# Kernel tuning notes

Hardware: AMD Instinct MI355X
Metric: run time of the kernel (lower is better)

Reference implementation:

```python
import jax, jax.numpy as jnp
import numpy as np

N = 50000      # nodes
E = 800000     # edges (before self loops)
IN_D = 128
HID = 128
OUT_D = 64
HEADS = 4
FH = HID // HEADS  # per-head feature dim
NEG_SLOPE = 0.2


def setup_inputs() -> dict:
    key = jax.random.key(0)
    ks = jax.random.split(key, 16)
    s = 0.05
    inp = {
        "x": jax.random.normal(ks[0], (N, IN_D), dtype=jnp.float32),
        "edge_index": jax.random.randint(ks[1], (2, E), 0, N, dtype=jnp.int32),
        "Wi": jax.random.normal(ks[2], (IN_D, HID), dtype=jnp.float32) * s,
        "bi": jnp.zeros((HID,), dtype=jnp.float32),
        "W0": jax.random.normal(ks[3], (HID, HID), dtype=jnp.float32) * s,
        "as0": jax.random.normal(ks[4], (HEADS, FH), dtype=jnp.float32) * s,
        "ad0": jax.random.normal(ks[5], (HEADS, FH), dtype=jnp.float32) * s,
        "b0": jnp.zeros((HID,), dtype=jnp.float32),
        "W1": jax.random.normal(ks[6], (HID, HID), dtype=jnp.float32) * s,
        "as1": jax.random.normal(ks[7], (HEADS, FH), dtype=jnp.float32) * s,
        "ad1": jax.random.normal(ks[8], (HEADS, FH), dtype=jnp.float32) * s,
        "b1": jnp.zeros((HID,), dtype=jnp.float32),
        "Wo": jax.random.normal(ks[9], (HID, OUT_D), dtype=jnp.float32) * s,
        "bo": jnp.zeros((OUT_D,), dtype=jnp.float32),
    }
    return inp


def _gat_layer(h, src, dst, W, a_src, a_dst, b):
    # h: [N, HID]; src/dst: [E'] (with self loops)
    hp = (h @ W).reshape(N, HEADS, FH)               # projected per-head features
    al_s = jnp.einsum('nhf,hf->nh', hp, a_src)       # [N, H]
    al_d = jnp.einsum('nhf,hf->nh', hp, a_dst)
    e = jax.nn.leaky_relu(al_s[src] + al_d[dst], NEG_SLOPE)  # [E', H]
    # neighbor softmax over incoming edges of each dst node (stable)
    m = jax.ops.segment_max(e, dst, num_segments=N)
    m = jnp.where(jnp.isfinite(m), m, 0.0)
    num = jnp.exp(e - m[dst])
    den = jax.ops.segment_sum(num, dst, num_segments=N)
    coef = num / (den[dst] + 1e-16)                  # [E', H]
    out = jax.ops.segment_sum(coef[:, :, None] * hp[src], dst, num_segments=N)
    return out.reshape(N, HID) + b


def reference(x, edge_index, Wi, bi, W0, as0, ad0, b0, W1, as1, ad1, b1, Wo, bo):
    # add self loops (PyG GATConv default)
    loop = jnp.arange(N, dtype=edge_index.dtype)
    src = jnp.concatenate([edge_index[0], loop])
    dst = jnp.concatenate([edge_index[1], loop])

    h = jax.nn.relu(x @ Wi + bi)
    # layer 0 (dropout = identity in eval)
    h = h + jax.nn.relu(_gat_layer(h, src, dst, W0, as0, ad0, b0))
    # layer 1
    h = h + jax.nn.relu(_gat_layer(h, src, dst, W1, as1, ad1, b1))
    return h @ Wo + bo
```

## Files before the change

kernel.cpp:

```cpp
#include <hip/hip_runtime.h>
#include <hip/hip_bf16.h>


__device__ __forceinline__ float lrelu(float x){ return x > 0.f ? x : 0.2f * x; }

typedef __attribute__((ext_vector_type(8))) short bf16x8;
typedef __attribute__((ext_vector_type(4))) float f32x4;

__device__ __forceinline__ ushort f2bf(float f){
    union { __hip_bfloat16 b; ushort u; } cv;
    cv.b = __float2bfloat16(f);
    return cv.u;
}
__device__ __forceinline__ float bf2f(short u){
    union { uint i; float f; } c;
    c.i = ((uint)(ushort)u) << 16;
    return c.f;
}

constexpr int CAP = 64;
constexpr int BUCKET_CAP = 8192;
constexpr int P1_EDGES = 2048;

__global__ __launch_bounds__(256) void bin_edges_kernel(
    const int* __restrict__ ei, int* __restrict__ gcur, int2* __restrict__ binned, int E, int N)
{
    __shared__ int hist[256], offs[256], gpos[256];
    __shared__ int2 stag[P1_EDGES];
    __shared__ int wsum[4];
    int tid = threadIdx.x;
    hist[tid] = 0;
    __syncthreads();

    int base = blockIdx.x * P1_EDGES;
    int srcv[8], dstv[8], rk[8];
    #pragma unroll
    for (int j = 0; j < 8; j++){
        int e = base + j * 256 + tid;
        if (e < E + N){
            int s, d;
            if (e < E){ s = ei[e]; d = ei[E + e]; } else { s = e - E; d = s; }
            srcv[j] = s; dstv[j] = d;
            rk[j] = atomicAdd(&hist[d >> 8], 1);
        } else dstv[j] = -1;
    }
    __syncthreads();

    int lane = tid & 63, wid = tid >> 6;
    int v = hist[tid];
    int x = v;
    #pragma unroll
    for (int o = 1; o < 64; o <<= 1){ int t = __shfl_up(x, o); if (lane >= o) x += t; }
    if (lane == 63) wsum[wid] = x;
    __syncthreads();
    int woff = 0;
    for (int w2 = 0; w2 < wid; w2++) woff += wsum[w2];
    offs[tid] = woff + x - v;
    __syncthreads();

    #pragma unroll
    for (int j = 0; j < 8; j++){
        if (dstv[j] >= 0){
            int b = dstv[j] >> 8;
            stag[offs[b] + rk[j]] = make_int2(srcv[j], dstv[j]);
        }
    }
    if (hist[tid] > 0) gpos[tid] = atomicAdd(&gcur[tid], hist[tid]);
    __syncthreads();

    int nE = offs[255] + hist[255];
    for (int i = tid; i < nE; i += 256){
        int2 p = stag[i];
        int b = p.y >> 8;
        int idx = gpos[b] + (i - offs[b]);
        if (idx < BUCKET_CAP) binned[(size_t)b * BUCKET_CAP + idx] = p;
    }
}

__global__ __launch_bounds__(256) void build_slots_kernel(
    const int* __restrict__ gcur, const int2* __restrict__ binned,
    int* __restrict__ cnt, int* __restrict__ slots, int N)
{
    __shared__ int cnt_l[256];
    __shared__ int slots_l[256][CAP];
    int tid = threadIdx.x;
    int b = blockIdx.x;
    cnt_l[tid] = 0;
    __syncthreads();

    int ne = gcur[b]; if (ne > BUCKET_CAP) ne = BUCKET_CAP;
    const int2* bp = binned + (size_t)b * BUCKET_CAP;
    for (int i = tid; i < ne; i += 256){
        int2 p = bp[i];
        int ld = p.y & 255;
        int pos = atomicAdd(&cnt_l[ld], 1);
        if (pos < CAP) slots_l[ld][pos] = p.x;
    }
    __syncthreads();

    int node = b * 256 + tid;
    if (node < N) cnt[node] = min(cnt_l[tid], CAP);
    for (int j = tid; j < 256 * CAP; j += 256){
        int n2 = b * 256 + (j >> 6);
        if (n2 < N) slots[(size_t)n2 * CAP + (j & 63)] = slots_l[j >> 6][j & 63];
    }
}

__global__ void wcast_all_kernel(const float* __restrict__ Wi, const float* __restrict__ W0,
                                 const float* __restrict__ W1, const float* __restrict__ Wo,
                                 ushort* __restrict__ ti, ushort* __restrict__ t0,
                                 ushort* __restrict__ t1, ushort* __restrict__ to_){
    int i = blockIdx.x * 256 + threadIdx.x;
    if (i < 16384){
        int k = i >> 7, n = i & 127;        ti[n * 128 + k] = f2bf(Wi[i]);
    } else if (i < 32768){
        int j = i - 16384; int k = j >> 7, n = j & 127;  t0[n * 128 + k] = f2bf(W0[j]);
    } else if (i < 49152){
        int j = i - 32768; int k = j >> 7, n = j & 127;  t1[n * 128 + k] = f2bf(W1[j]);
    } else if (i < 57344){
        int j = i - 49152; int k = j / 64, n = j % 64;   to_[n * 128 + k] = f2bf(Wo[j]);
    }
}

template<int NCOL, bool RELU, bool BIAS, bool BF16OUT, bool LOGITS>
__global__ __launch_bounds__(256) void mfma_matmul_kernel(
    const float* __restrict__ A,
    const ushort* __restrict__ Wt,
    const float* __restrict__ bias,
    void* __restrict__ Cv,
    const float* __restrict__ as_, const float* __restrict__ ad_,
    float* __restrict__ als, float* __restrict__ ald, int M)
{
    constexpr int NT = NCOL / 16;
    __shared__ ushort Ws[NCOL][136];
    int tid = threadIdx.x;
    for (int i = tid * 8; i < NCOL * 128; i += 256 * 8){
        int r = i >> 7, c = i & 127;
        *(uint4*)&Ws[r][c] = *(const uint4*)&Wt[i];
    }
    __syncthreads();

    int lane = tid & 63, wave = tid >> 6;
    int r15 = lane & 15;
    int ko  = (lane >> 4) * 8;
    int row  = blockIdx.x * 64 + wave * 16 + r15;
    int rowc = row < M ? row : M - 1;
    const float* Arow = A + (size_t)rowc * 128;

    f32x4 acc[NT];
    #pragma unroll
    for (int t = 0; t < NT; t++) acc[t] = (f32x4){0.f, 0.f, 0.f, 0.f};

    #pragma unroll
    for (int kt = 0; kt < 4; ++kt){
        float4 a0 = *(const float4*)&Arow[kt * 32 + ko];
        float4 a1 = *(const float4*)&Arow[kt * 32 + ko + 4];
        bf16x8 af;
        af[0] = f2bf(a0.x); af[1] = f2bf(a0.y); af[2] = f2bf(a0.z); af[3] = f2bf(a0.w);
        af[4] = f2bf(a1.x); af[5] = f2bf(a1.y); af[6] = f2bf(a1.z); af[7] = f2bf(a1.w);
        #pragma unroll
        for (int t = 0; t < NT; t++){
            bf16x8 bf = *(const bf16x8*)&Ws[t * 16 + r15][kt * 32 + ko];
            acc[t] = __builtin_amdgcn_mfma_f32_16x16x32_bf16(af, bf, acc[t], 0, 0, 0);
        }
    }

    int oc    = lane & 15;
    int orow0 = blockIdx.x * 64 + wave * 16 + (lane >> 4) * 4;
    #pragma unroll
    for (int t = 0; t < NT; t++){
        int ocol = t * 16 + oc;
        float bv = BIAS ? bias[ocol] : 0.f;
        #pragma unroll
        for (int rg = 0; rg < 4; rg++){
            int orow = orow0 + rg;
            if (orow < M){
                float v = acc[t][rg] + bv;
                if (RELU) v = fmaxf(v, 0.f);
                if (BF16OUT) ((ushort*)Cv)[(size_t)orow * NCOL + ocol] = f2bf(v);
                else         ((float*)Cv) [(size_t)orow * NCOL + ocol] = v;
            }
        }
    }

    if (LOGITS){
        float sva[4][4], svd[4][4];
        #pragma unroll
        for (int hh = 0; hh < 4; hh++){
            float as0v = as_[hh*32 + oc],      ad0v = ad_[hh*32 + oc];
            float as1v = as_[hh*32 + 16 + oc], ad1v = ad_[hh*32 + 16 + oc];
            #pragma unroll
            for (int rg = 0; rg < 4; rg++){
                sva[hh][rg] = acc[2*hh][rg] * as0v + acc[2*hh+1][rg] * as1v;
                svd[hh][rg] = acc[2*hh][rg] * ad0v + acc[2*hh+1][rg] * ad1v;
            }
        }
        #pragma unroll
        for (int o = 1; o < 16; o <<= 1){
            #pragma unroll
            for (int hh = 0; hh < 4; hh++)
                #pragma unroll
                for (int rg = 0; rg < 4; rg++){
                    sva[hh][rg] += __shfl_xor(sva[hh][rg], o);
                    svd[hh][rg] += __shfl_xor(svd[hh][rg], o);
                }
        }
        if (oc < 4){
            #pragma unroll
            for (int rg = 0; rg < 4; rg++){
                int orow = orow0 + rg;
                if (orow < M){
                    float va = (oc & 2) ? ((oc & 1) ? sva[3][rg] : sva[2][rg])
                                        : ((oc & 1) ? sva[1][rg] : sva[0][rg]);
                    float vd = (oc & 2) ? ((oc & 1) ? svd[3][rg] : svd[2][rg])
                                        : ((oc & 1) ? svd[1][rg] : svd[0][rg]);
                    als[orow * 4 + oc] = va;
                    ald[orow * 4 + oc] = vd;
                }
            }
        }
    }
}

__global__ __launch_bounds__(256) void gat_aggregate_kernel(
    const int* __restrict__ cnt, const int* __restrict__ slots,
    const ushort* __restrict__ hp, const float* __restrict__ als,
    const float* __restrict__ ald, const float* __restrict__ bias,
    float* __restrict__ h, int n)
{
    __shared__ float num_s[4][CAP * 5];
    __shared__ int   src_s[4][CAP];
    int wid = threadIdx.x >> 6;
    int lane = threadIdx.x & 63;
    int node = blockIdx.x * 4 + wid;
    float* nums = num_s[wid];
    int*   srcs = src_s[wid];

    int deg = 0;
    float4 aldv = make_float4(0.f,0.f,0.f,0.f);
    if (node < n){
        deg = cnt[node];
        if (deg > CAP) deg = CAP;
        aldv = *(const float4*)&ald[node * 4];
    }

    float m0=-1e30f, m1=-1e30f, m2=-1e30f, m3=-1e30f;
    if (lane < deg){
        int s = slots[node * CAP + lane];
        srcs[lane] = s;
        float4 av = *(const float4*)&als[s * 4];
        m0 = lrelu(av.x + aldv.x);
        m1 = lrelu(av.y + aldv.y);
        m2 = lrelu(av.z + aldv.z);
        m3 = lrelu(av.w + aldv.w);
        nums[lane*5+0]=m0; nums[lane*5+1]=m1; nums[lane*5+2]=m2; nums[lane*5+3]=m3;
    }
    #pragma unroll
    for (int o = 1; o < 64; o <<= 1){
        m0=fmaxf(m0,__shfl_xor(m0,o)); m1=fmaxf(m1,__shfl_xor(m1,o));
        m2=fmaxf(m2,__shfl_xor(m2,o)); m3=fmaxf(m3,__shfl_xor(m3,o));
    }
    __syncthreads();

    float d0=0.f,d1=0.f,d2=0.f,d3=0.f;
    if (lane < deg){
        d0 = __expf(nums[lane*5+0]-m0);
        d1 = __expf(nums[lane*5+1]-m1);
        d2 = __expf(nums[lane*5+2]-m2);
        d3 = __expf(nums[lane*5+3]-m3);
        nums[lane*5+0]=d0; nums[lane*5+1]=d1; nums[lane*5+2]=d2; nums[lane*5+3]=d3;
    }
    #pragma unroll
    for (int o = 1; o < 64; o <<= 1){
        d0+=__shfl_xor(d0,o); d1+=__shfl_xor(d1,o);
        d2+=__shfl_xor(d2,o); d3+=__shfl_xor(d3,o);
    }
    float inv0=1.f/(d0+1e-16f), inv1=1.f/(d1+1e-16f);
    float inv2=1.f/(d2+1e-16f), inv3=1.f/(d3+1e-16f);
    __syncthreads();

    int er = lane >> 4;
    int fg = (lane & 15) * 8;
    int head = (lane & 15) >> 2;
    float inv = (head & 2) ? ((head & 1) ? inv3 : inv2)
                           : ((head & 1) ? inv1 : inv0);
    float a0=0.f,a1=0.f,a2=0.f,a3=0.f,a4=0.f,a5=0.f,a6=0.f,a7=0.f;
    for (int i = 0; i < deg; i += 4){
        int e = i + er;
        bool v = e < deg;
        int ec = v ? e : 0;
        int s = srcs[ec];
        float c = nums[ec*5 + head] * inv;
        c = v ? c : 0.f;
        bf16x8 hv = *(const bf16x8*)&hp[(size_t)s * 128 + fg];
        a0 = fmaf(c, bf2f(hv[0]), a0);
        a1 = fmaf(c, bf2f(hv[1]), a1);
        a2 = fmaf(c, bf2f(hv[2]), a2);
        a3 = fmaf(c, bf2f(hv[3]), a3);
        a4 = fmaf(c, bf2f(hv[4]), a4);
        a5 = fmaf(c, bf2f(hv[5]), a5);
        a6 = fmaf(c, bf2f(hv[6]), a6);
        a7 = fmaf(c, bf2f(hv[7]), a7);
    }
    a0 += __shfl_xor(a0,16); a0 += __shfl_xor(a0,32);
    a1 += __shfl_xor(a1,16); a1 += __shfl_xor(a1,32);
    a2 += __shfl_xor(a2,16); a2 += __shfl_xor(a2,32);
    a3 += __shfl_xor(a3,16); a3 += __shfl_xor(a3,32);
    a4 += __shfl_xor(a4,16); a4 += __shfl_xor(a4,32);
    a5 += __shfl_xor(a5,16); a5 += __shfl_xor(a5,32);
    a6 += __shfl_xor(a6,16); a6 += __shfl_xor(a6,32);
    a7 += __shfl_xor(a7,16); a7 += __shfl_xor(a7,32);

    if (node < n){
        float sA = (er & 2) ? ((er & 1) ? a6 : a4) : ((er & 1) ? a2 : a0);
        float sB = (er & 2) ? ((er & 1) ? a7 : a5) : ((er & 1) ? a3 : a1);
        int f2 = fg + er * 2;
        float r0 = fmaxf(sA + bias[f2],     0.f);
        float r1 = fmaxf(sB + bias[f2 + 1], 0.f);
        float* hp2 = &h[(size_t)node * 128 + f2];
        float2 old = *(float2*)hp2;
        *(float2*)hp2 = make_float2(old.x + r0, old.y + r1);
    }
}

extern "C" void kernel_launch(void* const* d_in, const int* in_sizes, int n_in,
                              void* d_out, int out_size, void* d_ws, size_t ws_size,
                              hipStream_t stream)
{
    const float* x   = (const float*)d_in[0];
    const int*   ei  = (const int*)d_in[1];
    const float* Wi  = (const float*)d_in[2];
    const float* bi  = (const float*)d_in[3];
    const float* W0  = (const float*)d_in[4];
    const float* as0 = (const float*)d_in[5];
    const float* ad0 = (const float*)d_in[6];
    const float* b0  = (const float*)d_in[7];
    const float* W1  = (const float*)d_in[8];
    const float* as1 = (const float*)d_in[9];
    const float* ad1 = (const float*)d_in[10];
    const float* b1  = (const float*)d_in[11];
    const float* Wo  = (const float*)d_in[12];
    const float* bo  = (const float*)d_in[13];
    float* out = (float*)d_out;

    int N = in_sizes[0] / 128;
    int E = in_sizes[1] / 2;
    int EN = E + N;
    int NB = (N + 255) >> 8;

    char* w = (char*)d_ws;
    float*  h     = (float*)w;  w += (size_t)N * 128 * 4;
    ushort* hpb   = (ushort*)w; w += (size_t)N * 128 * 2;
    float*  als   = (float*)w;  w += (size_t)N * 4 * 4;
    float*  ald   = (float*)w;  w += (size_t)N * 4 * 4;
    int*    cnt   = (int*)w;    w += (size_t)N * 4;
    w = (char*)(((uintptr_t)w + 255) & ~(uintptr_t)255);
    int*    slots = (int*)w;    w += (size_t)N * CAP * 4;
    w = (char*)(((uintptr_t)w + 255) & ~(uintptr_t)255);
    int*    gcur  = (int*)w;    w += 256 * 4;
    w = (char*)(((uintptr_t)w + 255) & ~(uintptr_t)255);
    int2*   binned= (int2*)w;   w += (size_t)NB * BUCKET_CAP * 8;
    w = (char*)(((uintptr_t)w + 255) & ~(uintptr_t)255);
    ushort* wt_i  = (ushort*)w; w += (size_t)128 * 128 * 2;
    ushort* wt_0  = (ushort*)w; w += (size_t)128 * 128 * 2;
    ushort* wt_1  = (ushort*)w; w += (size_t)128 * 128 * 2;
    ushort* wt_o  = (ushort*)w; w += (size_t)64  * 128 * 2;

    hipMemsetAsync(gcur, 0, 256 * 4, stream);
    bin_edges_kernel<<<(EN + P1_EDGES - 1) / P1_EDGES, 256, 0, stream>>>(ei, gcur, binned, E, N);
    build_slots_kernel<<<NB, 256, 0, stream>>>(gcur, binned, cnt, slots, N);

    wcast_all_kernel<<<224, 256, 0, stream>>>(Wi, W0, W1, Wo, wt_i, wt_0, wt_1, wt_o);

    int mgrid = (N + 63) / 64;
    int agrid = (N + 3) / 4;

    mfma_matmul_kernel<128, true, true, false, false><<<mgrid, 256, 0, stream>>>(
        x, wt_i, bi, h, nullptr, nullptr, nullptr, nullptr, N);

    mfma_matmul_kernel<128, false, false, true, true><<<mgrid, 256, 0, stream>>>(
        h, wt_0, nullptr, hpb, as0, ad0, als, ald, N);
    gat_aggregate_kernel<<<agrid, 256, 0, stream>>>(cnt, slots, hpb, als, ald, b0, h, N);

    mfma_matmul_kernel<128, false, false, true, true><<<mgrid, 256, 0, stream>>>(
        h, wt_1, nullptr, hpb, as1, ad1, als, ald, N);
    gat_aggregate_kernel<<<agrid, 256, 0, stream>>>(cnt, slots, hpb, als, ald, b1, h, N);

    mfma_matmul_kernel<64, false, true, false, false><<<mgrid, 256, 0, stream>>>(
        h, wt_o, bo, out, nullptr, nullptr, nullptr, nullptr, N);
}
```

Before: 184.6 us.

## Split each node's GAT aggregation across two wavefronts by feature half

Measured after the change: 263.9 us. 42.9% more time.

```diff
diff --git a/kernel.cpp b/kernel.cpp
--- a/kernel.cpp
+++ b/kernel.cpp
@@ -232,7 +232,8 @@
     __shared__ int   src_s[4][CAP];
     int wid = threadIdx.x >> 6;
     int lane = threadIdx.x & 63;
-    int node = blockIdx.x * 4 + wid;
+    int node = blockIdx.x * 2 + (wid >> 1);
+    int half = wid & 1;
     float* nums = num_s[wid];
     int*   srcs = src_s[wid];
 
@@ -260,7 +261,6 @@
         m0=fmaxf(m0,__shfl_xor(m0,o)); m1=fmaxf(m1,__shfl_xor(m1,o));
         m2=fmaxf(m2,__shfl_xor(m2,o)); m3=fmaxf(m3,__shfl_xor(m3,o));
     }
-    __syncthreads();
 
     float d0=0.f,d1=0.f,d2=0.f,d3=0.f;
     if (lane < deg){
@@ -277,22 +277,22 @@
     }
     float inv0=1.f/(d0+1e-16f), inv1=1.f/(d1+1e-16f);
     float inv2=1.f/(d2+1e-16f), inv3=1.f/(d3+1e-16f);
-    __syncthreads();
-
-    int er = lane >> 4;
-    int fg = (lane & 15) * 8;
-    int head = (lane & 15) >> 2;
-    float inv = (head & 2) ? ((head & 1) ? inv3 : inv2)
-                           : ((head & 1) ? inv1 : inv0);
+
+    int er = lane >> 3;
+    int li = lane & 7;
+    int FG = half * 64 + li * 8;
+    int head = half * 2 + (li >> 2);
+    float inv = half ? ((li & 4) ? inv3 : inv2)
+                     : ((li & 4) ? inv1 : inv0);
     float a0=0.f,a1=0.f,a2=0.f,a3=0.f,a4=0.f,a5=0.f,a6=0.f,a7=0.f;
-    for (int i = 0; i < deg; i += 4){
+    for (int i = 0; i < deg; i += 8){
         int e = i + er;
         bool v = e < deg;
         int ec = v ? e : 0;
         int s = srcs[ec];
         float c = nums[ec*5 + head] * inv;
         c = v ? c : 0.f;
-        bf16x8 hv = *(const bf16x8*)&hp[(size_t)s * 128 + fg];
+        bf16x8 hv = *(const bf16x8*)&hp[(size_t)s * 128 + FG];
         a0 = fmaf(c, bf2f(hv[0]), a0);
         a1 = fmaf(c, bf2f(hv[1]), a1);
         a2 = fmaf(c, bf2f(hv[2]), a2);
@@ -302,24 +302,26 @@
         a6 = fmaf(c, bf2f(hv[6]), a6);
         a7 = fmaf(c, bf2f(hv[7]), a7);
     }
-    a0 += __shfl_xor(a0,16); a0 += __shfl_xor(a0,32);
-    a1 += __shfl_xor(a1,16); a1 += __shfl_xor(a1,32);
-    a2 += __shfl_xor(a2,16); a2 += __shfl_xor(a2,32);
-    a3 += __shfl_xor(a3,16); a3 += __shfl_xor(a3,32);
-    a4 += __shfl_xor(a4,16); a4 += __shfl_xor(a4,32);
-    a5 += __shfl_xor(a5,16); a5 += __shfl_xor(a5,32);
-    a6 += __shfl_xor(a6,16); a6 += __shfl_xor(a6,32);
-    a7 += __shfl_xor(a7,16); a7 += __shfl_xor(a7,32);
+    a0 += __shfl_xor(a0,8); a0 += __shfl_xor(a0,16); a0 += __shfl_xor(a0,32);
+    a1 += __shfl_xor(a1,8); a1 += __shfl_xor(a1,16); a1 += __shfl_xor(a1,32);
+    a2 += __shfl_xor(a2,8); a2 += __shfl_xor(a2,16); a2 += __shfl_xor(a2,32);
+    a3 += __shfl_xor(a3,8); a3 += __shfl_xor(a3,16); a3 += __shfl_xor(a3,32);
+    a4 += __shfl_xor(a4,8); a4 += __shfl_xor(a4,16); a4 += __shfl_xor(a4,32);
+    a5 += __shfl_xor(a5,8); a5 += __shfl_xor(a5,16); a5 += __shfl_xor(a5,32);
+    a6 += __shfl_xor(a6,8); a6 += __shfl_xor(a6,16); a6 += __shfl_xor(a6,32);
+    a7 += __shfl_xor(a7,8); a7 += __shfl_xor(a7,16); a7 += __shfl_xor(a7,32);
 
     if (node < n){
-        float sA = (er & 2) ? ((er & 1) ? a6 : a4) : ((er & 1) ? a2 : a0);
-        float sB = (er & 2) ? ((er & 1) ? a7 : a5) : ((er & 1) ? a3 : a1);
-        int f2 = fg + er * 2;
-        float r0 = fmaxf(sA + bias[f2],     0.f);
-        float r1 = fmaxf(sB + bias[f2 + 1], 0.f);
-        float* hp2 = &h[(size_t)node * 128 + f2];
-        float2 old = *(float2*)hp2;
-        *(float2*)hp2 = make_float2(old.x + r0, old.y + r1);
+        float t0 = (er & 1) ? a1 : a0;
+        float t1 = (er & 1) ? a3 : a2;
+        float t2 = (er & 1) ? a5 : a4;
+        float t3 = (er & 1) ? a7 : a6;
+        float u0 = (er & 2) ? t1 : t0;
+        float u1 = (er & 2) ? t3 : t2;
+        float val = (er & 4) ? u1 : u0;
+        int f = FG + er;
+        float r = fmaxf(val + bias[f], 0.f);
+        h[(size_t)node * 128 + f] += r;
     }
 }
 
@@ -373,7 +375,7 @@
     wcast_all_kernel<<<224, 256, 0, stream>>>(Wi, W0, W1, Wo, wt_i, wt_0, wt_1, wt_o);
 
     int mgrid = (N + 63) / 64;
-    int agrid = (N + 3) / 4;
+    int agrid = (N + 1) / 2;
 
     mfma_matmul_kernel<128, true, true, false, false><<<mgrid, 256, 0, stream>>>(
         x, wt_i, bi, h, nullptr, nullptr, nullptr, nullptr, N);
```
